# Optimization experiments

Measured on AMD Instinct MI355X. Metric: run time of the kernel, lower is better.

## Reference

```python
import jax, jax.numpy as jnp
import numpy as np


def setup_inputs() -> dict:
    key = jax.random.key(0)
    k1, k2, k3 = jax.random.split(key, 3)
    B, S, D = 128, 1024, 64
    return {
        "q": jax.random.normal(k1, (B, S, D), dtype=jnp.float32),
        "k": jax.random.normal(k2, (B, S, D), dtype=jnp.float32),
        "v": jax.random.normal(k3, (B, S, D), dtype=jnp.float32),
    }


def reference(q, k, v):
    # Faithful to the torch module: NO 1/sqrt(d) scaling.
    # Chunking over batch dim in the original is math-equivalent to full bmm.
    scores = jnp.einsum("bsd,btd->bst", q, k)  # [B, S, S]
    attn = jax.nn.softmax(scores, axis=-1)
    return jnp.einsum("bst,btd->bsd", attn, v)  # [B, S, D]
```

## Files before the change

### kernel.cpp

```cpp
#include <hip/hip_runtime.h>
#include <math.h>

namespace {

typedef _Float16 half8 __attribute__((ext_vector_type(8)));
typedef float floatx4 __attribute__((ext_vector_type(4)));

constexpr int kS   = 1024;
constexpr int kD   = 64;
constexpr int kPad = 72;
constexpr float kLog2e = 1.4426950408889634f;

union H4 { _Float16 h[4]; uint2 u2; };

__device__ __forceinline__ float fast_exp2(float x) {
#if __has_builtin(__builtin_amdgcn_exp2f)
  return __builtin_amdgcn_exp2f(x);
#else
  return exp2f(x);
#endif
}

__device__ __forceinline__ float fast_rcp(float x) {
#if __has_builtin(__builtin_amdgcn_rcpf)
  return __builtin_amdgcn_rcpf(x);
#else
  return 1.0f / x;
#endif
}

__global__ __launch_bounds__(256, 3)
void fa_mfma_kernel(const float* __restrict__ qg, const float* __restrict__ kg,
                    const float* __restrict__ vg, float* __restrict__ og) {
  __shared__ __align__(16) _Float16 sK [64][kPad];
  __shared__ __align__(16) _Float16 sVt[64][kPad];
  __shared__ __align__(16) _Float16 sP [128][kPad];

  const int tid  = threadIdx.x;
  const int lane = tid & 63;
  const int w    = __builtin_amdgcn_readfirstlane(tid >> 6);
  const int quad = lane >> 4;
  const int r    = lane & 15;

  const int blk = blockIdx.x;
  const int s   = blk >> 3;
  const int b   = (blk & 7) + 8 * (s & 15);
  const int qbase = (s >> 4) * 128;

  const float* qb = qg + (size_t)b * kS * kD;
  const float* kb = kg + (size_t)b * kS * kD;
  const float* vb = vg + (size_t)b * kS * kD;
  float*       ob = og + (size_t)b * kS * kD;

  half8 fqh[2][2], fql[2][2];
#pragma unroll
  for (int ntq = 0; ntq < 2; ++ntq)
#pragma unroll
    for (int ks = 0; ks < 2; ++ks) {
      const float* src =
          qb + (size_t)(qbase + w * 32 + ntq * 16 + r) * kD + ks * 32 + quad * 8;
      float4 a = ((const float4*)src)[0];
      float4 c = ((const float4*)src)[1];
      float f[8] = {a.x, a.y, a.z, a.w, c.x, c.y, c.z, c.w};
#pragma unroll
      for (int j = 0; j < 8; ++j) {
        float x = f[j] * kLog2e;
        _Float16 h = (_Float16)x;
        fqh[ntq][ks][j] = h;
        fql[ntq][ks][j] = (_Float16)(x - (float)h);
      }
    }

  float m_i[2] = {-INFINITY, -INFINITY}, l_i[2] = {0.f, 0.f};
  floatx4 O[2][4];
#pragma unroll
  for (int a = 0; a < 2; ++a)
#pragma unroll
    for (int c = 0; c < 4; ++c) O[a][c] = floatx4{0.f, 0.f, 0.f, 0.f};

  const int krow = tid >> 2, kc0 = (tid & 3) * 16;
  const int vkey = tid & 63, vd0 = (tid >> 6) * 16;
  float4 kbuf[4], vbuf[4];
  {
    const float4* ksrc = (const float4*)(kb + (size_t)krow * kD + kc0);
    const float4* vsrc = (const float4*)(vb + (size_t)vkey * kD + vd0);
#pragma unroll
    for (int g = 0; g < 4; ++g) { kbuf[g] = ksrc[g]; vbuf[g] = vsrc[g]; }
  }

  for (int kt = 0; kt < kS / 64; ++kt) {
    __syncthreads();
#pragma unroll
    for (int g = 0; g < 4; ++g) {
      float t[4] = {kbuf[g].x, kbuf[g].y, kbuf[g].z, kbuf[g].w};
      H4 hk;
#pragma unroll
      for (int j = 0; j < 4; ++j) hk.h[j] = (_Float16)t[j];
      *(uint2*)&sK[krow][kc0 + g * 4] = hk.u2;
    }
#pragma unroll
    for (int g = 0; g < 4; ++g) {
      float t[4] = {vbuf[g].x, vbuf[g].y, vbuf[g].z, vbuf[g].w};
#pragma unroll
      for (int j = 0; j < 4; ++j) sVt[vd0 + g * 4 + j][vkey] = (_Float16)t[j];
    }
    {
      const int ktn = (kt + 1) & 15;
      const float4* ksrc =
          (const float4*)(kb + (size_t)(ktn * 64 + krow) * kD + kc0);
      const float4* vsrc =
          (const float4*)(vb + (size_t)(ktn * 64 + vkey) * kD + vd0);
#pragma unroll
      for (int g = 0; g < 4; ++g) { kbuf[g] = ksrc[g]; vbuf[g] = vsrc[g]; }
    }
    __syncthreads();

    floatx4 S[2][4];
#pragma unroll
    for (int mt = 0; mt < 4; ++mt) {
      half8 fk0 = *(const half8*)&sK[mt * 16 + r][0 * 32 + quad * 8];
      half8 fk1 = *(const half8*)&sK[mt * 16 + r][1 * 32 + quad * 8];
#pragma unroll
      for (int ntq = 0; ntq < 2; ++ntq) {
        floatx4 ah = {0.f, 0.f, 0.f, 0.f}, al = {0.f, 0.f, 0.f, 0.f};
        ah = __builtin_amdgcn_mfma_f32_16x16x32_f16(fk0, fqh[ntq][0], ah, 0, 0, 0);
        ah = __builtin_amdgcn_mfma_f32_16x16x32_f16(fk1, fqh[ntq][1], ah, 0, 0, 0);
        al = __builtin_amdgcn_mfma_f32_16x16x32_f16(fk0, fql[ntq][0], al, 0, 0, 0);
        al = __builtin_amdgcn_mfma_f32_16x16x32_f16(fk1, fql[ntq][1], al, 0, 0, 0);
        S[ntq][mt] = ah + al;
      }
    }

    float alpha[2];
#pragma unroll
    for (int ntq = 0; ntq < 2; ++ntq) {
      float tm = -INFINITY;
#pragma unroll
      for (int mt = 0; mt < 4; ++mt)
#pragma unroll
        for (int j = 0; j < 4; ++j) tm = fmaxf(tm, S[ntq][mt][j]);
      tm = fmaxf(tm, __shfl_xor(tm, 16, 64));
      tm = fmaxf(tm, __shfl_xor(tm, 32, 64));
      const float mn = fmaxf(m_i[ntq], tm);
      alpha[ntq] = fast_exp2(m_i[ntq] - mn);
      float rs = 0.f;
#pragma unroll
      for (int mt = 0; mt < 4; ++mt) {
        H4 hp;
#pragma unroll
        for (int j = 0; j < 4; ++j) {
          float pj = fast_exp2(S[ntq][mt][j] - mn);
          rs += pj;
          hp.h[j] = (_Float16)pj;
        }
        *(uint2*)&sP[w * 32 + ntq * 16 + r][mt * 16 + quad * 4] = hp.u2;
      }
      rs += __shfl_xor(rs, 16, 64);
      rs += __shfl_xor(rs, 32, 64);
      l_i[ntq] = l_i[ntq] * alpha[ntq] + rs;
      m_i[ntq] = mn;
    }

#pragma unroll
    for (int mtq = 0; mtq < 2; ++mtq)
#pragma unroll
      for (int j = 0; j < 4; ++j) {
        const float a = __shfl(alpha[mtq], quad * 4 + j, 64);
#pragma unroll
        for (int nd = 0; nd < 4; ++nd) O[mtq][nd][j] *= a;
      }

#pragma unroll
    for (int ks = 0; ks < 2; ++ks) {
      half8 fp0 = *(const half8*)&sP[w * 32 + 0 * 16 + r][ks * 32 + quad * 8];
      half8 fp1 = *(const half8*)&sP[w * 32 + 1 * 16 + r][ks * 32 + quad * 8];
#pragma unroll
      for (int nd = 0; nd < 4; ++nd) {
        half8 fv = *(const half8*)&sVt[nd * 16 + r][ks * 32 + quad * 8];
        O[0][nd] = __builtin_amdgcn_mfma_f32_16x16x32_f16(fp0, fv, O[0][nd], 0, 0, 0);
        O[1][nd] = __builtin_amdgcn_mfma_f32_16x16x32_f16(fp1, fv, O[1][nd], 0, 0, 0);
      }
    }
  }

#pragma unroll
  for (int mtq = 0; mtq < 2; ++mtq)
#pragma unroll
    for (int j = 0; j < 4; ++j) {
      const float lrow = __shfl(l_i[mtq], quad * 4 + j, 64);
      const float linv = fast_rcp(lrow);
      float* dst =
          ob + (size_t)(qbase + w * 32 + mtq * 16 + quad * 4 + j) * kD + r;
#pragma unroll
      for (int nd = 0; nd < 4; ++nd) dst[nd * 16] = O[mtq][nd][j] * linv;
    }
}

}

extern "C" void kernel_launch(void* const* d_in, const int* in_sizes, int n_in,
                              void* d_out, int out_size, void* d_ws, size_t ws_size,
                              hipStream_t stream) {
  const float* q = (const float*)d_in[0];
  const float* k = (const float*)d_in[1];
  const float* v = (const float*)d_in[2];
  float* out = (float*)d_out;

  fa_mfma_kernel<<<dim3(1024), 256, 0, stream>>>(q, k, v, out);
}
```

Measured before the change: 202.2 us.

## Load K straight from global into MFMA fragments and double-buffer V in LDS

Drops the shared-memory staging of K: each wave now reads its K fragments directly from global memory and converts them to fp16 in registers. V is double-buffered in LDS, with the next tile loaded and transposed during the softmax, so each iteration needs only one barrier instead of two. With less LDS in use, the launch bounds now ask for 4 blocks per CU instead of 3. In exchange, every wave fetches the whole K tile, which multiplies K traffic from L2 by four. Those K loads also sit unprefetched directly ahead of the QK MFMAs, so their latency is exposed.

```diff
diff --git a/kernel.cpp b/kernel.cpp
--- a/kernel.cpp
+++ b/kernel.cpp
@@ -12,6 +12,7 @@
 constexpr float kLog2e = 1.4426950408889634f;
 
 union H4 { _Float16 h[4]; uint2 u2; };
+union H8 { _Float16 h[8]; half8 v; };
 
 __device__ __forceinline__ float fast_exp2(float x) {
 #if __has_builtin(__builtin_amdgcn_exp2f)
@@ -29,12 +30,11 @@
 #endif
 }
 
-__global__ __launch_bounds__(256, 3)
+__global__ __launch_bounds__(256, 4)
 void fa_mfma_kernel(const float* __restrict__ qg, const float* __restrict__ kg,
                     const float* __restrict__ vg, float* __restrict__ og) {
-  __shared__ __align__(16) _Float16 sK [64][kPad];
-  __shared__ __align__(16) _Float16 sVt[64][kPad];
-  __shared__ __align__(16) _Float16 sP [128][kPad];
+  __shared__ __align__(16) _Float16 sVt[2][64][kPad];
+  __shared__ __align__(16) _Float16 sP[128][kPad];
 
   const int tid  = threadIdx.x;
   const int lane = tid & 63;
@@ -47,10 +47,10 @@
   const int b   = (blk & 7) + 8 * (s & 15);
   const int qbase = (s >> 4) * 128;
 
-  const float* qb = qg + (size_t)b * kS * kD;
-  const float* kb = kg + (size_t)b * kS * kD;
-  const float* vb = vg + (size_t)b * kS * kD;
-  float*       ob = og + (size_t)b * kS * kD;
+  const float* qp = qg + (size_t)b * kS * kD;
+  const float* kp = kg + (size_t)b * kS * kD;
+  const float* vp = vg + (size_t)b * kS * kD;
+  float*       op = og + (size_t)b * kS * kD;
 
   half8 fqh[2][2], fql[2][2];
 #pragma unroll
@@ -58,7 +58,7 @@
 #pragma unroll
     for (int ks = 0; ks < 2; ++ks) {
       const float* src =
-          qb + (size_t)(qbase + w * 32 + ntq * 16 + r) * kD + ks * 32 + quad * 8;
+          qp + (size_t)(qbase + w * 32 + ntq * 16 + r) * kD + ks * 32 + quad * 8;
       float4 a = ((const float4*)src)[0];
       float4 c = ((const float4*)src)[1];
       float f[8] = {a.x, a.y, a.z, a.w, c.x, c.y, c.z, c.w};
@@ -78,58 +78,60 @@
 #pragma unroll
     for (int c = 0; c < 4; ++c) O[a][c] = floatx4{0.f, 0.f, 0.f, 0.f};
 
-  const int krow = tid >> 2, kc0 = (tid & 3) * 16;
   const int vkey = tid & 63, vd0 = (tid >> 6) * 16;
-  float4 kbuf[4], vbuf[4];
+
   {
-    const float4* ksrc = (const float4*)(kb + (size_t)krow * kD + kc0);
-    const float4* vsrc = (const float4*)(vb + (size_t)vkey * kD + vd0);
-#pragma unroll
-    for (int g = 0; g < 4; ++g) { kbuf[g] = ksrc[g]; vbuf[g] = vsrc[g]; }
+    float4 vbuf[4];
+#pragma unroll
+    for (int g = 0; g < 4; ++g)
+      vbuf[g] = *(const float4*)(vp + (size_t)vkey * kD + vd0 + g * 4);
+#pragma unroll
+    for (int g = 0; g < 4; ++g) {
+      float t[4] = {vbuf[g].x, vbuf[g].y, vbuf[g].z, vbuf[g].w};
+#pragma unroll
+      for (int j = 0; j < 4; ++j)
+        sVt[0][vd0 + g * 4 + j][vkey] = (_Float16)t[j];
+    }
   }
 
   for (int kt = 0; kt < kS / 64; ++kt) {
     __syncthreads();
-#pragma unroll
-    for (int g = 0; g < 4; ++g) {
-      float t[4] = {kbuf[g].x, kbuf[g].y, kbuf[g].z, kbuf[g].w};
-      H4 hk;
-#pragma unroll
-      for (int j = 0; j < 4; ++j) hk.h[j] = (_Float16)t[j];
-      *(uint2*)&sK[krow][kc0 + g * 4] = hk.u2;
-    }
-#pragma unroll
-    for (int g = 0; g < 4; ++g) {
-      float t[4] = {vbuf[g].x, vbuf[g].y, vbuf[g].z, vbuf[g].w};
-#pragma unroll
-      for (int j = 0; j < 4; ++j) sVt[vd0 + g * 4 + j][vkey] = (_Float16)t[j];
-    }
-    {
-      const int ktn = (kt + 1) & 15;
-      const float4* ksrc =
-          (const float4*)(kb + (size_t)(ktn * 64 + krow) * kD + kc0);
-      const float4* vsrc =
-          (const float4*)(vb + (size_t)(ktn * 64 + vkey) * kD + vd0);
-#pragma unroll
-      for (int g = 0; g < 4; ++g) { kbuf[g] = ksrc[g]; vbuf[g] = vsrc[g]; }
-    }
-    __syncthreads();
 
     floatx4 S[2][4];
 #pragma unroll
     for (int mt = 0; mt < 4; ++mt) {
-      half8 fk0 = *(const half8*)&sK[mt * 16 + r][0 * 32 + quad * 8];
-      half8 fk1 = *(const half8*)&sK[mt * 16 + r][1 * 32 + quad * 8];
+      const float* krow =
+          kp + (size_t)(kt * 64 + mt * 16 + r) * kD + quad * 8;
+      float4 a0 = ((const float4*)krow)[0];
+      float4 a1 = ((const float4*)(krow + 4))[0];
+      float4 b0 = ((const float4*)(krow + 32))[0];
+      float4 b1 = ((const float4*)(krow + 36))[0];
+      H8 fk0, fk1;
+      {
+        float t0[8] = {a0.x, a0.y, a0.z, a0.w, a1.x, a1.y, a1.z, a1.w};
+        float t1[8] = {b0.x, b0.y, b0.z, b0.w, b1.x, b1.y, b1.z, b1.w};
+#pragma unroll
+        for (int j = 0; j < 8; ++j) {
+          fk0.h[j] = (_Float16)t0[j];
+          fk1.h[j] = (_Float16)t1[j];
+        }
+      }
 #pragma unroll
       for (int ntq = 0; ntq < 2; ++ntq) {
         floatx4 ah = {0.f, 0.f, 0.f, 0.f}, al = {0.f, 0.f, 0.f, 0.f};
-        ah = __builtin_amdgcn_mfma_f32_16x16x32_f16(fk0, fqh[ntq][0], ah, 0, 0, 0);
-        ah = __builtin_amdgcn_mfma_f32_16x16x32_f16(fk1, fqh[ntq][1], ah, 0, 0, 0);
-        al = __builtin_amdgcn_mfma_f32_16x16x32_f16(fk0, fql[ntq][0], al, 0, 0, 0);
-        al = __builtin_amdgcn_mfma_f32_16x16x32_f16(fk1, fql[ntq][1], al, 0, 0, 0);
+        ah = __builtin_amdgcn_mfma_f32_16x16x32_f16(fk0.v, fqh[ntq][0], ah, 0, 0, 0);
+        ah = __builtin_amdgcn_mfma_f32_16x16x32_f16(fk1.v, fqh[ntq][1], ah, 0, 0, 0);
+        al = __builtin_amdgcn_mfma_f32_16x16x32_f16(fk0.v, fql[ntq][0], al, 0, 0, 0);
+        al = __builtin_amdgcn_mfma_f32_16x16x32_f16(fk1.v, fql[ntq][1], al, 0, 0, 0);
         S[ntq][mt] = ah + al;
       }
     }
+
+    const int ktn = (kt + 1) & 15;
+    float4 vbuf[4];
+#pragma unroll
+    for (int g = 0; g < 4; ++g)
+      vbuf[g] = *(const float4*)(vp + (size_t)(ktn * 64 + vkey) * kD + vd0 + g * 4);
 
     float alpha[2];
 #pragma unroll
@@ -162,6 +164,14 @@
     }
 
 #pragma unroll
+    for (int g = 0; g < 4; ++g) {
+      float t[4] = {vbuf[g].x, vbuf[g].y, vbuf[g].z, vbuf[g].w};
+#pragma unroll
+      for (int j = 0; j < 4; ++j)
+        sVt[(kt + 1) & 1][vd0 + g * 4 + j][vkey] = (_Float16)t[j];
+    }
+
+#pragma unroll
     for (int mtq = 0; mtq < 2; ++mtq)
 #pragma unroll
       for (int j = 0; j < 4; ++j) {
@@ -176,7 +186,7 @@
       half8 fp1 = *(const half8*)&sP[w * 32 + 1 * 16 + r][ks * 32 + quad * 8];
 #pragma unroll
       for (int nd = 0; nd < 4; ++nd) {
-        half8 fv = *(const half8*)&sVt[nd * 16 + r][ks * 32 + quad * 8];
+        half8 fv = *(const half8*)&sVt[kt & 1][nd * 16 + r][ks * 32 + quad * 8];
         O[0][nd] = __builtin_amdgcn_mfma_f32_16x16x32_f16(fp0, fv, O[0][nd], 0, 0, 0);
         O[1][nd] = __builtin_amdgcn_mfma_f32_16x16x32_f16(fp1, fv, O[1][nd], 0, 0, 0);
       }
@@ -190,7 +200,7 @@
       const float lrow = __shfl(l_i[mtq], quad * 4 + j, 64);
       const float linv = fast_rcp(lrow);
       float* dst =
-          ob + (size_t)(qbase + w * 32 + mtq * 16 + quad * 4 + j) * kD + r;
+          op + (size_t)(qbase + w * 32 + mtq * 16 + quad * 4 + j) * kD + r;
 #pragma unroll
       for (int nd = 0; nd < 4; ++nd) dst[nd * 16] = O[mtq][nd][j] * linv;
     }
```

Result: slower. 315.1 us (+55.9%).
